# Optimization experiments

Measured on AMD Instinct MI355X. Metric: run time of the kernel, lower is better.

The kernel has to match this reference:

```python
import jax, jax.numpy as jnp
import numpy as np

BS, L, D = 128, 256, 512
H, DK = 2, 256  # heads, head dim
EPS_BN = 1e-5


def _lin(x, W, b):
    # torch Linear: W is (out, in)
    return jnp.einsum('...i,oi->...o', x, W) + b


def _bn(x, g, b, m, v):
    # eval-mode BatchNorm over channel axis = last axis of x
    return (x - m) * (g * jax.lax.rsqrt(v + EPS_BN)) + b


def setup_inputs() -> dict:
    key = jax.random.key(0)
    ks = iter(jax.random.split(key, 64))
    rn = lambda shape, s=0.02: jax.random.normal(next(ks), shape, dtype=jnp.float32) * s
    inp = {}
    inp['cap_emb'] = jax.random.normal(next(ks), (BS, L, D), dtype=jnp.float32)
    inp['lengths'] = jax.random.randint(next(ks), (BS,), 1, L + 1, dtype=jnp.int64 if jax.config.jax_enable_x64 else jnp.int32)
    # GA linears q,k,v
    for nm in ('Wq', 'Wk', 'Wv'):
        inp[nm] = rn((D, D))
    for nm in ('bq', 'bk', 'bv'):
        inp[nm] = rn((D,))
    inp['Wfq'] = rn((DK, DK)); inp['bfq'] = rn((DK,))
    inp['Wfk'] = rn((DK, DK)); inp['bfk'] = rn((DK,))
    inp['Wfg'] = rn((2 * DK, DK)); inp['bfg'] = rn((2 * DK,))
    # BatchNorm params (eval running stats)
    for pre in ('bn1', 'bn2', 'bn3'):
        inp[pre + '_g'] = 1.0 + rn((D,), 0.1)
        inp[pre + '_b'] = rn((D,), 0.1)
        inp[pre + '_m'] = rn((D,), 0.1)
        inp[pre + '_v'] = jax.random.uniform(next(ks), (D,), minval=0.5, maxval=1.5, dtype=jnp.float32)
    # Conv1d weights, torch layout (out, in, k)
    inp['Wc2'] = rn((D, D, 2)); inp['bc2'] = rn((D,))
    inp['Wc3'] = rn((D, D, 3)); inp['bc3'] = rn((D,))
    # MLP 512 -> 1024 -> 512
    inp['Wm1'] = rn((2 * D, D)); inp['bm1'] = rn((2 * D,))
    inp['Wm2'] = rn((D, 2 * D)); inp['bm2'] = rn((D,))
    return inp


def _forward(cap_emb, Wq, bq, Wk, bk, Wv, bv, Wfq, bfq, Wfk, bfk, Wfg, bfg,
             bn1_g, bn1_b, bn1_m, bn1_v, Wc2, bc2, bn2_g, bn2_b, bn2_m, bn2_v,
             Wc3, bc3, bn3_g, bn3_b, bn3_m, bn3_v, Wm1, bm1, Wm2, bm2, lengths):
    bs, seq, dim = cap_emb.shape
    # ---- GA: gated self-attention ----
    def split_heads(x):
        return x.reshape(bs, seq, H, DK).transpose(0, 2, 1, 3)  # [bs,h,seq,dk]
    q = split_heads(_lin(cap_emb, Wq, bq))
    k = split_heads(_lin(cap_emb, Wk, bk))
    v = split_heads(_lin(cap_emb, Wv, bv))
    G = _lin(q, Wfq, bfq) * _lin(k, Wfk, bfk)
    M = jax.nn.sigmoid(_lin(G, Wfg, bfg))  # [bs,h,seq,2*dk]
    qg = q * M[..., :DK]
    kg = k * M[..., DK:]
    # torch.div(..., rounding_mode='floor') == elementwise floor of scaled scores
    scores = jnp.floor(jnp.einsum('bhqd,bhkd->bhqk', qg, kg) / jnp.sqrt(jnp.float32(DK)))
    p_attn = jax.nn.softmax(scores, axis=-1)
    x = jnp.einsum('bhqk,bhkd->bhqd', p_attn, v)
    x = x.transpose(0, 2, 1, 3).reshape(bs, seq, dim)
    # BN over features (eval), dropout is identity in eval mode
    ga_emb = cap_emb + _bn(x, bn1_g, bn1_b, bn1_m, bn1_v)
    # ---- dual conv1d branches ----
    xc = cap_emb.transpose(0, 2, 1)  # [bs, D, L]
    dn = ('NCW', 'OIW', 'NCW')
    c2 = jax.lax.conv_general_dilated(xc, Wc2, window_strides=(2,), padding='VALID', dimension_numbers=dn) + bc2[None, :, None]
    c3 = jax.lax.conv_general_dilated(xc, Wc3, window_strides=(3,), padding='VALID', dimension_numbers=dn) + bc3[None, :, None]
    f2 = jax.nn.relu(_bn(c2.transpose(0, 2, 1), bn2_g, bn2_b, bn2_m, bn2_v))
    f3 = jax.nn.relu(_bn(c3.transpose(0, 2, 1), bn3_g, bn3_b, bn3_m, bn3_v))
    ga_jw = jnp.concatenate([ga_emb, f2, f3], axis=1)
    # ---- residual MLP (dropout identity in eval) ----
    hid = jax.nn.relu(_lin(ga_jw, Wm1, bm1))
    tex_emb = _lin(hid, Wm2, bm2) + ga_jw
    # ---- length-indexed gather ----
    idx = lengths.astype(jnp.int32) - 1
    out = tex_emb[jnp.arange(bs), idx]  # [bs, D]
    # l2norm
    norm = jnp.sqrt(jnp.sum(out * out, axis=-1, keepdims=True)) + 1e-8
    return out / norm


def reference(cap_emb, lengths, Wq, bq, Wk, bk, Wv, bv, Wfq, bfq, Wfk, bfk, Wfg, bfg,
              bn1_g, bn1_b, bn1_m, bn1_v, Wc2, bc2, bn2_g, bn2_b, bn2_m, bn2_v,
              Wc3, bc3, bn3_g, bn3_b, bn3_m, bn3_v, Wm1, bm1, Wm2, bm2):
    return _forward(cap_emb, Wq, bq, Wk, bk, Wv, bv, Wfq, bfq, Wfk, bfk, Wfg, bfg,
                    bn1_g, bn1_b, bn1_m, bn1_v, Wc2, bc2, bn2_g, bn2_b, bn2_m, bn2_v,
                    Wc3, bc3, bn3_g, bn3_b, bn3_m, bn3_v, Wm1, bm1, Wm2, bm2, lengths)
```

## Files before the change

### kernel.cpp

```cpp
#include <hip/hip_runtime.h>
#include <math.h>


typedef short bf16x8 __attribute__((ext_vector_type(8)));
typedef float f32x4 __attribute__((ext_vector_type(4)));
typedef short short4v __attribute__((ext_vector_type(4)));

__device__ __forceinline__ short f2bf(float x) {
    union { float f; unsigned u; } c; c.f = x;
    unsigned r = c.u + 0x7FFFu + ((c.u >> 16) & 1u);
    return (short)(r >> 16);
}
__device__ __forceinline__ float bf2f(short h) {
    union { float f; unsigned u; } c; c.u = ((unsigned)(unsigned short)h) << 16;
    return c.f;
}
__device__ __forceinline__ void glds16(const void* g, void* l) {
    __builtin_amdgcn_global_load_lds(
        (const __attribute__((address_space(1))) void*)g,
        (__attribute__((address_space(3))) void*)l, 16, 0, 0);
}

struct CastArgs {
    const float* src[3];
    short* dst[3];
    int n4[3];
};
__global__ __launch_bounds__(256) void cast_multi(CastArgs a)
{
    const int j = blockIdx.y;
    const float4* s = (const float4*)a.src[j];
    short* d = a.dst[j];
    const int n4 = a.n4[j];
    for (int i = blockIdx.x * 256 + threadIdx.x; i < n4; i += gridDim.x * 256) {
        float4 x = s[i];
        short4v h;
        h.x = f2bf(x.x); h.y = f2bf(x.y); h.z = f2bf(x.z); h.w = f2bf(x.w);
        *(short4v*)&d[i * 4] = h;
    }
}

__global__ __launch_bounds__(256)
void compose2(const float* __restrict__ Wq, const float* __restrict__ bq,
              const float* __restrict__ Wfq, const float* __restrict__ bfq,
              const float* __restrict__ Wk, const float* __restrict__ bk,
              const float* __restrict__ Wfk, const float* __restrict__ bfk,
              short* __restrict__ WaB, float* __restrict__ ba,
              short* __restrict__ WbB, float* __restrict__ bb)
{
    __shared__ float fq[256];
    __shared__ float redc[256];
    const int op = blockIdx.x;
    const int h = op >> 8, o = op & 255;
    const int t = threadIdx.x;
    const bool second = (blockIdx.y == 1);
    const float* W  = second ? Wk  : Wq;
    const float* bv = second ? bk  : bq;
    const float* F  = second ? Wfk : Wfq;
    const float* bf = second ? bfk : bfq;
    short* WB   = second ? WbB : WaB;
    float* bout = second ? bb  : ba;

    fq[t] = F[o * 256 + t];
    redc[t] = fq[t] * bv[h * 256 + t];
    __syncthreads();
    for (int s = 128; s > 0; s >>= 1) {
        if (t < s) redc[t] += redc[t + s];
        __syncthreads();
    }
    if (t == 0) bout[op] = redc[0] + bf[o];
    float s0 = 0.f, s1 = 0.f;
    for (int d = 0; d < 256; ++d) {
        const float f = fq[d];
        const float* wr = W + (size_t)(h * 256 + d) * 512;
        s0 += f * wr[t];
        s1 += f * wr[t + 256];
    }
    const size_t ro = (size_t)op * 512;
    WB[ro + t] = f2bf(s0);
    WB[ro + 256 + t] = f2bf(s1);
}

__global__ __launch_bounds__(256, 2)
void gemm_g(const short* __restrict__ capB,
            const short* __restrict__ WaB, const short* __restrict__ WbB,
            const float* __restrict__ ba, const float* __restrict__ bb,
            short* __restrict__ Gbuf)
{
    __shared__ short lds[2][12288];
    const int tid = threadIdx.x;
    const int bm = blockIdx.y * 128;
    const int bn = blockIdx.x * 128;
    const int z = blockIdx.z;
    const short* B1 = WaB + (size_t)z * 256 * 512;
    const short* B2 = WbB + (size_t)z * 256 * 512;

    const int lane = tid & 63;
    const int wr = (tid >> 7) & 1, wc = (tid >> 6) & 1;
    const int fr = lane & 15, kc = lane >> 4;
    const int r0 = tid >> 2;
    const int e0 = (((tid & 3) ^ ((r0 >> 1) & 3))) * 8;
    const int kce = (kc ^ ((fr >> 1) & 3)) * 8;

    auto stage = [&](int ph, int k0) {
        short* b = lds[ph];
        glds16(capB + (size_t)(bm + r0) * 512 + k0 + e0,      b + tid * 8);
        glds16(capB + (size_t)(bm + r0 + 64) * 512 + k0 + e0, b + (tid + 256) * 8);
        glds16(B1 + (size_t)(bn + r0) * 512 + k0 + e0,        b + 4096 + tid * 8);
        glds16(B1 + (size_t)(bn + r0 + 64) * 512 + k0 + e0,   b + 4096 + (tid + 256) * 8);
        glds16(B2 + (size_t)(bn + r0) * 512 + k0 + e0,        b + 8192 + tid * 8);
        glds16(B2 + (size_t)(bn + r0 + 64) * 512 + k0 + e0,   b + 8192 + (tid + 256) * 8);
    };

    f32x4 acc1[4][4], acc2[4][4];
#pragma unroll
    for (int i = 0; i < 4; ++i)
#pragma unroll
        for (int j = 0; j < 4; ++j) {
            acc1[i][j] = (f32x4){0.f, 0.f, 0.f, 0.f};
            acc2[i][j] = (f32x4){0.f, 0.f, 0.f, 0.f};
        }

    stage(0, 0);
    __syncthreads();
    for (int s = 0; s < 16; ++s) {
        if (s + 1 < 16) stage((s + 1) & 1, (s + 1) * 32);
        const short* b = lds[s & 1];
        bf16x8 ah[4], bh[4];
#pragma unroll
        for (int i = 0; i < 4; ++i)
            ah[i] = *(const bf16x8*)&b[(wr * 64 + i * 16 + fr) * 32 + kce];
#pragma unroll
        for (int i = 0; i < 4; ++i)
            bh[i] = *(const bf16x8*)&b[4096 + (wc * 64 + i * 16 + fr) * 32 + kce];
#pragma unroll
        for (int mi = 0; mi < 4; ++mi)
#pragma unroll
            for (int ni = 0; ni < 4; ++ni)
                acc1[mi][ni] = __builtin_amdgcn_mfma_f32_16x16x32_bf16(ah[mi], bh[ni], acc1[mi][ni], 0, 0, 0);
#pragma unroll
        for (int i = 0; i < 4; ++i)
            bh[i] = *(const bf16x8*)&b[8192 + (wc * 64 + i * 16 + fr) * 32 + kce];
#pragma unroll
        for (int mi = 0; mi < 4; ++mi)
#pragma unroll
            for (int ni = 0; ni < 4; ++ni)
                acc2[mi][ni] = __builtin_amdgcn_mfma_f32_16x16x32_bf16(ah[mi], bh[ni], acc2[mi][ni], 0, 0, 0);
        __syncthreads();
    }

#pragma unroll
    for (int mi = 0; mi < 4; ++mi) {
#pragma unroll
        for (int ni = 0; ni < 4; ++ni) {
#pragma unroll
            for (int r = 0; r < 4; ++r) {
                const int row = bm + wr * 64 + mi * 16 + kc * 4 + r;
                const int col = bn + wc * 64 + ni * 16 + fr;
                const float av  = acc1[mi][ni][r] + ba[z * 256 + col];
                const float lin = acc2[mi][ni][r] + bb[z * 256 + col];
                Gbuf[(size_t)row * 512 + z * 256 + col] = f2bf(lin * av);
            }
        }
    }
}

__global__ __launch_bounds__(256, 2)
void gemm_kg(const short* __restrict__ Gbuf,
             const short* __restrict__ Wfg2B, const float* __restrict__ bias,
             const short* __restrict__ capB,
             const short* __restrict__ WkB, const float* __restrict__ bk,
             const float* __restrict__ qg, float* __restrict__ scorep)
{
    __shared__ short lds[2][16384];
    __shared__ float sp[256];
    const int tid = threadIdx.x;
    const int bm = blockIdx.y * 128;
    const int bn = blockIdx.x * 128;
    const int z = blockIdx.z;
    const short* A1 = Gbuf + (size_t)z * 256;
    const short* B2 = WkB + (size_t)z * 256 * 512;

    const int lane = tid & 63;
    const int wr = (tid >> 7) & 1, wc = (tid >> 6) & 1;
    const int fr = lane & 15, kc = lane >> 4;
    const int r0 = tid >> 2;
    const int e0 = (((tid & 3) ^ ((r0 >> 1) & 3))) * 8;
    const int kce = (kc ^ ((fr >> 1) & 3)) * 8;

    auto stage = [&](int ph, int s) {
        short* b = lds[ph];
        const int k0 = s * 32;
        glds16(capB + (size_t)(bm + r0) * 512 + k0 + e0,      b + 8192 + tid * 8);
        glds16(capB + (size_t)(bm + r0 + 64) * 512 + k0 + e0, b + 8192 + (tid + 256) * 8);
        glds16(B2 + (size_t)(bn + r0) * 512 + k0 + e0,        b + 12288 + tid * 8);
        glds16(B2 + (size_t)(bn + r0 + 64) * 512 + k0 + e0,   b + 12288 + (tid + 256) * 8);
        if (s < 8) {
            glds16(A1 + (size_t)(bm + r0) * 512 + k0 + e0,        b + tid * 8);
            glds16(A1 + (size_t)(bm + r0 + 64) * 512 + k0 + e0,   b + (tid + 256) * 8);
            glds16(Wfg2B + (size_t)(bn + r0) * 256 + k0 + e0,     b + 4096 + tid * 8);
            glds16(Wfg2B + (size_t)(bn + r0 + 64) * 256 + k0 + e0, b + 4096 + (tid + 256) * 8);
        }
    };

    f32x4 acc1[4][4], acc2[4][4];
#pragma unroll
    for (int i = 0; i < 4; ++i)
#pragma unroll
        for (int j = 0; j < 4; ++j) {
            acc1[i][j] = (f32x4){0.f, 0.f, 0.f, 0.f};
            acc2[i][j] = (f32x4){0.f, 0.f, 0.f, 0.f};
        }

    stage(0, 0);
    __syncthreads();
    for (int s = 0; s < 16; ++s) {
        if (s + 1 < 16) stage((s + 1) & 1, s + 1);
        const short* b = lds[s & 1];
        bf16x8 ah[4], bh[4];
#pragma unroll
        for (int i = 0; i < 4; ++i)
            ah[i] = *(const bf16x8*)&b[8192 + (wr * 64 + i * 16 + fr) * 32 + kce];
#pragma unroll
        for (int i = 0; i < 4; ++i)
            bh[i] = *(const bf16x8*)&b[12288 + (wc * 64 + i * 16 + fr) * 32 + kce];
#pragma unroll
        for (int mi = 0; mi < 4; ++mi)
#pragma unroll
            for (int ni = 0; ni < 4; ++ni)
                acc2[mi][ni] = __builtin_amdgcn_mfma_f32_16x16x32_bf16(ah[mi], bh[ni], acc2[mi][ni], 0, 0, 0);
        if (s < 8) {
#pragma unroll
            for (int i = 0; i < 4; ++i)
                ah[i] = *(const bf16x8*)&b[(wr * 64 + i * 16 + fr) * 32 + kce];
#pragma unroll
            for (int i = 0; i < 4; ++i)
                bh[i] = *(const bf16x8*)&b[4096 + (wc * 64 + i * 16 + fr) * 32 + kce];
#pragma unroll
            for (int mi = 0; mi < 4; ++mi)
#pragma unroll
                for (int ni = 0; ni < 4; ++ni)
                    acc1[mi][ni] = __builtin_amdgcn_mfma_f32_16x16x32_bf16(ah[mi], bh[ni], acc1[mi][ni], 0, 0, 0);
        }
        __syncthreads();
    }

    float qgv[4];
    float pt[4][4];
    {
        const int b = bm >> 8;
#pragma unroll
        for (int ni = 0; ni < 4; ++ni)
            qgv[ni] = qg[b * 512 + z * 256 + bn + wc * 64 + ni * 16 + fr];
#pragma unroll
        for (int mi = 0; mi < 4; ++mi)
#pragma unroll
            for (int r = 0; r < 4; ++r) pt[mi][r] = 0.f;
    }

#pragma unroll
    for (int mi = 0; mi < 4; ++mi) {
#pragma unroll
        for (int ni = 0; ni < 4; ++ni) {
#pragma unroll
            for (int r = 0; r < 4; ++r) {
                const int col = bn + wc * 64 + ni * 16 + fr;
                const float v = acc1[mi][ni][r] + bias[col];
                const float e = acc2[mi][ni][r] + bk[z * 256 + col];
                const float kgv = e / (1.f + expf(-v));
                pt[mi][r] += kgv * qgv[ni];
            }
        }
    }

#pragma unroll
    for (int mi = 0; mi < 4; ++mi) {
#pragma unroll
        for (int r = 0; r < 4; ++r) {
            float p = pt[mi][r];
            p += __shfl_xor(p, 1);
            p += __shfl_xor(p, 2);
            p += __shfl_xor(p, 4);
            p += __shfl_xor(p, 8);
            if (fr == 0) {
                const int row_local = wr * 64 + mi * 16 + kc * 4 + r;
                sp[row_local * 2 + wc] = p;
            }
        }
    }
    __syncthreads();
    if (tid < 128) {
        const int row = bm + tid;
        const float s = sp[tid * 2] + sp[tid * 2 + 1];
        const int b = row >> 8, j = row & 255;
        scorep[((size_t)(b * 2 + z) * 256 + j) * 2 + blockIdx.x] = s;
    }
}

__global__ __launch_bounds__(256)
void qg_kernel(const float* __restrict__ cap,
               const short* __restrict__ Gbuf,
               const float* __restrict__ Wq, const float* __restrict__ bq,
               const float* __restrict__ Wfg, const float* __restrict__ bfg,
               const int* __restrict__ lengths, float* __restrict__ qg)
{
    __shared__ float cr[512];
    __shared__ float gs[256];
    const int b = blockIdx.x >> 1, h = blockIdx.x & 1;
    const int t = threadIdx.x;
    int r = lengths[b] - 1;
    if (r < 0) r = 0;
    if (r > 255) r = 255;
    const size_t base = ((size_t)b * 256 + r) * 512;
    cr[t] = cap[base + t];
    cr[t + 256] = cap[base + 256 + t];
    gs[t] = bf2f(Gbuf[base + h * 256 + t]);
    __syncthreads();
    const float4* wq4 = (const float4*)(Wq + (size_t)(h * 256 + t) * 512);
    float q = 0.f;
    for (int k4 = 0; k4 < 128; ++k4) {
        float4 w = wq4[k4];
        q += w.x * cr[k4 * 4 + 0] + w.y * cr[k4 * 4 + 1]
           + w.z * cr[k4 * 4 + 2] + w.w * cr[k4 * 4 + 3];
    }
    q += bq[h * 256 + t];
    const float4* w4 = (const float4*)(Wfg + (size_t)t * 256);
    float a = 0.f;
    for (int k4 = 0; k4 < 64; ++k4) {
        float4 w = w4[k4];
        a += w.x * gs[k4 * 4 + 0] + w.y * gs[k4 * 4 + 1]
           + w.z * gs[k4 * 4 + 2] + w.w * gs[k4 * 4 + 3];
    }
    a += bfg[t];
    qg[b * 512 + h * 256 + t] = q / (1.f + expf(-a));
}

__global__ __launch_bounds__(256)
void pbar_kernel(const float* __restrict__ scorep, const short* __restrict__ capB,
                 float* __restrict__ pbar)
{
    __shared__ float sc[512], red[512];
    const int b = blockIdx.y, cg = blockIdx.x;
    const int t = threadIdx.x;
#pragma unroll
    for (int i = 0; i < 2; ++i) {
        const int o = t + i * 256;
        const int h = o >> 8, j = o & 255;
        const size_t si = ((size_t)(b * 2 + h) * 256 + j) * 2;
        sc[o] = floorf((scorep[si] + scorep[si + 1]) * 0.0625f);
    }
    __syncthreads();
    red[t] = sc[t]; red[t + 256] = sc[t + 256];
    __syncthreads();
    for (int s = 128; s > 0; s >>= 1) {
        if (t < s) {
            red[t] = fmaxf(red[t], red[t + s]);
            red[256 + t] = fmaxf(red[256 + t], red[256 + t + s]);
        }
        __syncthreads();
    }
    const float mx0 = red[0], mx1 = red[256];
    __syncthreads();
    const float e0 = expf(sc[t] - mx0);
    const float e1 = expf(sc[t + 256] - mx1);
    red[t] = e0; red[t + 256] = e1;
    __syncthreads();
    for (int s = 128; s > 0; s >>= 1) {
        if (t < s) { red[t] += red[t + s]; red[256 + t] += red[256 + t + s]; }
        __syncthreads();
    }
    sc[t] = e0 / red[0];
    sc[t + 256] = e1 / red[256];
    __syncthreads();

    const int c = cg * 64 + (t & 63);
    const int jg = t >> 6;
    float a0 = 0.f, a1 = 0.f;
    for (int j = jg * 64; j < jg * 64 + 64; ++j) {
        const float cv = bf2f(capB[((size_t)(b * 256 + j)) * 512 + c]);
        a0 += sc[j] * cv;
        a1 += sc[256 + j] * cv;
    }
    red[t] = a0;
    __syncthreads();
    if (t < 64) {
        const float s0 = red[t] + red[t + 64] + red[t + 128] + red[t + 192];
        pbar[b * 1024 + cg * 64 + t] = s0;
    }
    __syncthreads();
    red[t] = a1;
    __syncthreads();
    if (t < 64) {
        const float s1 = red[t] + red[t + 64] + red[t + 128] + red[t + 192];
        pbar[b * 1024 + 512 + cg * 64 + t] = s1;
    }
}

__global__ __launch_bounds__(256)
void bnx_kernel(const float* __restrict__ pbar, const float* __restrict__ cap,
                const int* __restrict__ lengths,
                const float* __restrict__ Wv, const float* __restrict__ bv,
                const float* __restrict__ g1, const float* __restrict__ b1,
                const float* __restrict__ m1, const float* __restrict__ v1,
                float* __restrict__ xga)
{
    __shared__ float pb[1024];
    const int b = blockIdx.x;
    const int t = threadIdx.x;
    int r = lengths[b] - 1;
    if (r < 0) r = 0;
    if (r > 255) r = 255;
    const size_t base = ((size_t)b * 256 + r) * 512;
    pb[t] = pbar[b * 1024 + t];
    pb[t + 256] = pbar[b * 1024 + 256 + t];
    pb[t + 512] = pbar[b * 1024 + 512 + t];
    pb[t + 768] = pbar[b * 1024 + 768 + t];
    __syncthreads();
    float x0 = 0.f, x1 = 0.f;
    {
        const float4* w4 = (const float4*)(Wv + (size_t)t * 512);
        for (int k4 = 0; k4 < 128; ++k4) {
            float4 w = w4[k4];
            x0 += w.x * pb[k4 * 4 + 0] + w.y * pb[k4 * 4 + 1]
                + w.z * pb[k4 * 4 + 2] + w.w * pb[k4 * 4 + 3];
        }
        x0 += bv[t];
    }
    {
        const float4* w4 = (const float4*)(Wv + (size_t)(t + 256) * 512);
        for (int k4 = 0; k4 < 128; ++k4) {
            float4 w = w4[k4];
            x1 += w.x * pb[512 + k4 * 4 + 0] + w.y * pb[512 + k4 * 4 + 1]
                + w.z * pb[512 + k4 * 4 + 2] + w.w * pb[512 + k4 * 4 + 3];
        }
        x1 += bv[t + 256];
    }
    const int c0 = t, c1 = t + 256;
    const float s0 = g1[c0] / sqrtf(v1[c0] + 1e-5f);
    const float s1 = g1[c1] / sqrtf(v1[c1] + 1e-5f);
    xga[b * 512 + c0] = cap[base + c0] + (x0 - m1[c0]) * s0 + b1[c0];
    xga[b * 512 + c1] = cap[base + c1] + (x1 - m1[c1]) * s1 + b1[c1];
}

__global__ __launch_bounds__(256)
void mlp1(const float* __restrict__ xga, const float* __restrict__ W,
          const float* __restrict__ bias, float* __restrict__ hid)
{
    __shared__ float xs[16 * 512];
    const int r0 = blockIdx.y * 16;
    const int c0 = blockIdx.x * 64;
    for (int i = threadIdx.x; i < 2048; i += 256)
        ((float4*)xs)[i] = ((const float4*)(xga + (size_t)r0 * 512))[i];
    __syncthreads();
    const int col = c0 + (threadIdx.x & 63);
    const int rg = (threadIdx.x >> 6) * 4;
    float acc[4] = {0.f, 0.f, 0.f, 0.f};
    const float4* w4 = (const float4*)(W + (size_t)col * 512);
    for (int k4 = 0; k4 < 128; ++k4) {
        float4 w = w4[k4];
#pragma unroll
        for (int rr = 0; rr < 4; ++rr) {
            float4 x = *(const float4*)&xs[(rg + rr) * 512 + k4 * 4];
            acc[rr] += w.x * x.x + w.y * x.y + w.z * x.z + w.w * x.w;
        }
    }
    const float bb = bias[col];
#pragma unroll
    for (int rr = 0; rr < 4; ++rr)
        hid[(size_t)(r0 + rg + rr) * 1024 + col] = fmaxf(acc[rr] + bb, 0.f);
}

__global__ __launch_bounds__(256)
void mlp2(const float* __restrict__ hid, const float* __restrict__ W,
          const float* __restrict__ bias, const float* __restrict__ xga,
          float* __restrict__ tex)
{
    __shared__ float xs[16 * 1024];
    const int r0 = blockIdx.y * 16;
    const int c0 = blockIdx.x * 64;
    for (int i = threadIdx.x; i < 4096; i += 256)
        ((float4*)xs)[i] = ((const float4*)(hid + (size_t)r0 * 1024))[i];
    __syncthreads();
    const int col = c0 + (threadIdx.x & 63);
    const int rg = (threadIdx.x >> 6) * 4;
    float acc[4] = {0.f, 0.f, 0.f, 0.f};
    const float4* w4 = (const float4*)(W + (size_t)col * 1024);
    for (int k4 = 0; k4 < 256; ++k4) {
        float4 w = w4[k4];
#pragma unroll
        for (int rr = 0; rr < 4; ++rr) {
            float4 x = *(const float4*)&xs[(rg + rr) * 1024 + k4 * 4];
            acc[rr] += w.x * x.x + w.y * x.y + w.z * x.z + w.w * x.w;
        }
    }
    const float bb = bias[col];
#pragma unroll
    for (int rr = 0; rr < 4; ++rr) {
        const int row = r0 + rg + rr;
        tex[(size_t)row * 512 + col] = acc[rr] + bb + xga[(size_t)row * 512 + col];
    }
}

__global__ __launch_bounds__(256)
void norm_out(const float* __restrict__ tex, float* __restrict__ out)
{
    __shared__ float red[256];
    const int b = blockIdx.x;
    const int t = threadIdx.x;
    const float a = tex[b * 512 + t];
    const float c = tex[b * 512 + 256 + t];
    red[t] = a * a + c * c;
    __syncthreads();
    for (int s = 128; s > 0; s >>= 1) {
        if (t < s) red[t] += red[t + s];
        __syncthreads();
    }
    const float inv = 1.f / (sqrtf(red[0]) + 1e-8f);
    out[b * 512 + t] = a * inv;
    out[b * 512 + 256 + t] = c * inv;
}

extern "C" void kernel_launch(void* const* d_in, const int* in_sizes, int n_in,
                              void* d_out, int out_size, void* d_ws, size_t ws_size,
                              hipStream_t stream)
{
    const float* cap = (const float*)d_in[0];
    const int* lengths = (const int*)d_in[1];
    const float* Wq  = (const float*)d_in[2];
    const float* Wk  = (const float*)d_in[3];
    const float* Wv  = (const float*)d_in[4];
    const float* bq  = (const float*)d_in[5];
    const float* bk  = (const float*)d_in[6];
    const float* bv  = (const float*)d_in[7];
    const float* Wfq = (const float*)d_in[8];
    const float* bfq = (const float*)d_in[9];
    const float* Wfk = (const float*)d_in[10];
    const float* bfk = (const float*)d_in[11];
    const float* Wfg = (const float*)d_in[12];
    const float* bfg = (const float*)d_in[13];
    const float* g1  = (const float*)d_in[14];
    const float* b1  = (const float*)d_in[15];
    const float* m1  = (const float*)d_in[16];
    const float* v1  = (const float*)d_in[17];
    const float* Wm1 = (const float*)d_in[30];
    const float* bm1 = (const float*)d_in[31];
    const float* Wm2 = (const float*)d_in[32];
    const float* bm2 = (const float*)d_in[33];
    float* out = (float*)d_out;

    char* w = (char*)d_ws;
    const size_t MB = 1024 * 1024;
    short* capB = (short*)(w);
    short* Gbuf = (short*)(w + 32 * MB);
    char* wp = w + 64 * MB;
    short* WkB   = (short*)wp; wp += 524288;
    short* WaB   = (short*)wp; wp += 524288;
    short* WbB   = (short*)wp; wp += 524288;
    short* Wfg2B = (short*)wp; wp += 131072;
    float* ba     = (float*)wp; wp += 2048;
    float* bb     = (float*)wp; wp += 2048;
    float* qg     = (float*)wp; wp += 262144;
    float* scorep = (float*)wp; wp += 524288;
    float* pbar   = (float*)wp; wp += 524288;
    float* xga    = (float*)wp; wp += 262144;
    float* hid    = (float*)wp; wp += 524288;
    float* tex    = (float*)wp; wp += 262144;

    CastArgs ca;
    ca.src[0] = cap;          ca.dst[0] = capB;  ca.n4[0] = 4194304;
    ca.src[1] = Wk;           ca.dst[1] = WkB;   ca.n4[1] = 65536;
    ca.src[2] = Wfg + 65536;  ca.dst[2] = Wfg2B; ca.n4[2] = 16384;
    cast_multi<<<dim3(4096, 3), 256, 0, stream>>>(ca);

    compose2<<<dim3(512, 2), 256, 0, stream>>>(Wq, bq, Wfq, bfq, Wk, bk, Wfk, bfk,
                                               WaB, ba, WbB, bb);

    gemm_g<<<dim3(2, 256, 2), 256, 0, stream>>>(capB, WaB, WbB, ba, bb, Gbuf);

    qg_kernel<<<dim3(256), 256, 0, stream>>>(cap, Gbuf, Wq, bq, Wfg, bfg, lengths, qg);

    gemm_kg<<<dim3(2, 256, 2), 256, 0, stream>>>(Gbuf, Wfg2B, bfg + 256,
                                                 capB, WkB, bk, qg, scorep);

    pbar_kernel<<<dim3(8, 128), 256, 0, stream>>>(scorep, capB, pbar);
    bnx_kernel<<<dim3(128), 256, 0, stream>>>(pbar, cap, lengths, Wv, bv, g1, b1, m1, v1, xga);

    mlp1<<<dim3(16, 8), 256, 0, stream>>>(xga, Wm1, bm1, hid);
    mlp2<<<dim3(8, 8), 256, 0, stream>>>(hid, Wm2, bm2, xga, tex);
    norm_out<<<dim3(128), 256, 0, stream>>>(tex, out);
}
```

Baseline: 269.3 us.

## Fuse launches: merge prep, g-gemm with qg, pbar with bnx, MLP with norm

Cuts the pipeline from ten launches to five. The cast and weight-compose steps merge into one prep kernel. The qg computation runs as extra blocks inside the G GEMM and recomputes the needed G row itself from the composed weights, so it no longer waits on Gbuf. The pbar reduction is folded into the bnx kernel, now one block per batch. The two MLP layers and the l2 norm are fused into a single 32-block kernel, which removes the launch gaps and intermediate buffers but leaves much less parallelism in the pbar and MLP stages.

```diff
diff --git a/kernel.cpp b/kernel.cpp
--- a/kernel.cpp
+++ b/kernel.cpp
@@ -21,45 +21,42 @@
         (__attribute__((address_space(3))) void*)l, 16, 0, 0);
 }
 
-struct CastArgs {
+struct PrepArgs {
     const float* src[3];
     short* dst[3];
     int n4[3];
+    const float *Wq, *bq, *Wfq, *bfq, *Wk, *bk, *Wfk, *bfk;
+    short *WaB, *WbB;
+    float *ba, *bb;
 };
-__global__ __launch_bounds__(256) void cast_multi(CastArgs a)
+__global__ __launch_bounds__(256) void prep_kernel(PrepArgs a)
 {
-    const int j = blockIdx.y;
-    const float4* s = (const float4*)a.src[j];
-    short* d = a.dst[j];
-    const int n4 = a.n4[j];
-    for (int i = blockIdx.x * 256 + threadIdx.x; i < n4; i += gridDim.x * 256) {
-        float4 x = s[i];
-        short4v h;
-        h.x = f2bf(x.x); h.y = f2bf(x.y); h.z = f2bf(x.z); h.w = f2bf(x.w);
-        *(short4v*)&d[i * 4] = h;
-    }
-}
-
-__global__ __launch_bounds__(256)
-void compose2(const float* __restrict__ Wq, const float* __restrict__ bq,
-              const float* __restrict__ Wfq, const float* __restrict__ bfq,
-              const float* __restrict__ Wk, const float* __restrict__ bk,
-              const float* __restrict__ Wfk, const float* __restrict__ bfk,
-              short* __restrict__ WaB, float* __restrict__ ba,
-              short* __restrict__ WbB, float* __restrict__ bb)
-{
+    const int y = blockIdx.y;
+    const int t = threadIdx.x;
+    if (y < 3) {
+        const float4* s = (const float4*)a.src[y];
+        short* d = a.dst[y];
+        const int n4 = a.n4[y];
+        for (int i = blockIdx.x * 256 + t; i < n4; i += gridDim.x * 256) {
+            float4 x = s[i];
+            short4v h;
+            h.x = f2bf(x.x); h.y = f2bf(x.y); h.z = f2bf(x.z); h.w = f2bf(x.w);
+            *(short4v*)&d[i * 4] = h;
+        }
+        return;
+    }
+    if (blockIdx.x >= 512) return;
     __shared__ float fq[256];
     __shared__ float redc[256];
     const int op = blockIdx.x;
     const int h = op >> 8, o = op & 255;
-    const int t = threadIdx.x;
-    const bool second = (blockIdx.y == 1);
-    const float* W  = second ? Wk  : Wq;
-    const float* bv = second ? bk  : bq;
-    const float* F  = second ? Wfk : Wfq;
-    const float* bf = second ? bfk : bfq;
-    short* WB   = second ? WbB : WaB;
-    float* bout = second ? bb  : ba;
+    const bool second = (y == 4);
+    const float* W  = second ? a.Wk  : a.Wq;
+    const float* bv = second ? a.bk  : a.bq;
+    const float* F  = second ? a.Wfk : a.Wfq;
+    const float* bf = second ? a.bfk : a.bfq;
+    short* WB   = second ? a.WbB : a.WaB;
+    float* bout = second ? a.bb  : a.ba;
 
     fq[t] = F[o * 256 + t];
     redc[t] = fq[t] * bv[h * 256 + t];
@@ -81,17 +78,72 @@
     WB[ro + 256 + t] = f2bf(s1);
 }
 
-__global__ __launch_bounds__(256, 2)
-void gemm_g(const short* __restrict__ capB,
-            const short* __restrict__ WaB, const short* __restrict__ WbB,
-            const float* __restrict__ ba, const float* __restrict__ bb,
-            short* __restrict__ Gbuf)
+__global__ __launch_bounds__(256)
+void gemm_g_qg(const short* __restrict__ capB,
+               const short* __restrict__ WaB, const short* __restrict__ WbB,
+               const float* __restrict__ ba, const float* __restrict__ bb,
+               short* __restrict__ Gbuf,
+               const float* __restrict__ cap,
+               const float* __restrict__ Wq, const float* __restrict__ bq,
+               const float* __restrict__ Wfg, const float* __restrict__ bfg,
+               const int* __restrict__ lengths, float* __restrict__ qg)
 {
     __shared__ short lds[2][12288];
     const int tid = threadIdx.x;
-    const int bm = blockIdx.y * 128;
-    const int bn = blockIdx.x * 128;
-    const int z = blockIdx.z;
+
+    if (blockIdx.x < 256) {
+        float* cr = (float*)&lds[0][0];
+        float* gs = cr + 512;
+        const int b = blockIdx.x >> 1, h = blockIdx.x & 1;
+        const int t = tid;
+        int r = lengths[b] - 1;
+        if (r < 0) r = 0;
+        if (r > 255) r = 255;
+        const size_t base = ((size_t)b * 256 + r) * 512;
+        cr[t] = cap[base + t];
+        cr[t + 256] = cap[base + 256 + t];
+        __syncthreads();
+        {
+            const bf16x8* wa8 = (const bf16x8*)(WaB + (size_t)(h * 256 + t) * 512);
+            const bf16x8* wb8 = (const bf16x8*)(WbB + (size_t)(h * 256 + t) * 512);
+            float sa = 0.f, sb = 0.f;
+            for (int k8 = 0; k8 < 64; ++k8) {
+                bf16x8 wa = wa8[k8];
+                bf16x8 wb = wb8[k8];
+#pragma unroll
+                for (int j = 0; j < 8; ++j) {
+                    const float c = cr[k8 * 8 + j];
+                    sa += bf2f(wa[j]) * c;
+                    sb += bf2f(wb[j]) * c;
+                }
+            }
+            gs[t] = (sb + bb[h * 256 + t]) * (sa + ba[h * 256 + t]);
+        }
+        __syncthreads();
+        const float4* wq4 = (const float4*)(Wq + (size_t)(h * 256 + t) * 512);
+        float q = 0.f;
+        for (int k4 = 0; k4 < 128; ++k4) {
+            float4 w = wq4[k4];
+            q += w.x * cr[k4 * 4 + 0] + w.y * cr[k4 * 4 + 1]
+               + w.z * cr[k4 * 4 + 2] + w.w * cr[k4 * 4 + 3];
+        }
+        q += bq[h * 256 + t];
+        const float4* w4 = (const float4*)(Wfg + (size_t)t * 256);
+        float a = 0.f;
+        for (int k4 = 0; k4 < 64; ++k4) {
+            float4 w = w4[k4];
+            a += w.x * gs[k4 * 4 + 0] + w.y * gs[k4 * 4 + 1]
+               + w.z * gs[k4 * 4 + 2] + w.w * gs[k4 * 4 + 3];
+        }
+        a += bfg[t];
+        qg[b * 512 + h * 256 + t] = q / (1.f + expf(-a));
+        return;
+    }
+
+    const int gid = blockIdx.x - 256;
+    const int bn = (gid & 1) * 128;
+    const int bm = ((gid >> 1) & 255) * 128;
+    const int z = gid >> 9;
     const short* B1 = WaB + (size_t)z * 256 * 512;
     const short* B2 = WbB + (size_t)z * 256 * 512;
 
@@ -298,49 +350,15 @@
 }
 
 __global__ __launch_bounds__(256)
-void qg_kernel(const float* __restrict__ cap,
-               const short* __restrict__ Gbuf,
-               const float* __restrict__ Wq, const float* __restrict__ bq,
-               const float* __restrict__ Wfg, const float* __restrict__ bfg,
-               const int* __restrict__ lengths, float* __restrict__ qg)
+void pbar_bnx(const float* __restrict__ scorep, const short* __restrict__ capB,
+              const float* __restrict__ cap, const int* __restrict__ lengths,
+              const float* __restrict__ Wv, const float* __restrict__ bv,
+              const float* __restrict__ g1, const float* __restrict__ b1,
+              const float* __restrict__ m1, const float* __restrict__ v1,
+              float* __restrict__ xga)
 {
-    __shared__ float cr[512];
-    __shared__ float gs[256];
-    const int b = blockIdx.x >> 1, h = blockIdx.x & 1;
-    const int t = threadIdx.x;
-    int r = lengths[b] - 1;
-    if (r < 0) r = 0;
-    if (r > 255) r = 255;
-    const size_t base = ((size_t)b * 256 + r) * 512;
-    cr[t] = cap[base + t];
-    cr[t + 256] = cap[base + 256 + t];
-    gs[t] = bf2f(Gbuf[base + h * 256 + t]);
-    __syncthreads();
-    const float4* wq4 = (const float4*)(Wq + (size_t)(h * 256 + t) * 512);
-    float q = 0.f;
-    for (int k4 = 0; k4 < 128; ++k4) {
-        float4 w = wq4[k4];
-        q += w.x * cr[k4 * 4 + 0] + w.y * cr[k4 * 4 + 1]
-           + w.z * cr[k4 * 4 + 2] + w.w * cr[k4 * 4 + 3];
-    }
-    q += bq[h * 256 + t];
-    const float4* w4 = (const float4*)(Wfg + (size_t)t * 256);
-    float a = 0.f;
-    for (int k4 = 0; k4 < 64; ++k4) {
-        float4 w = w4[k4];
-        a += w.x * gs[k4 * 4 + 0] + w.y * gs[k4 * 4 + 1]
-           + w.z * gs[k4 * 4 + 2] + w.w * gs[k4 * 4 + 3];
-    }
-    a += bfg[t];
-    qg[b * 512 + h * 256 + t] = q / (1.f + expf(-a));
-}
-
-__global__ __launch_bounds__(256)
-void pbar_kernel(const float* __restrict__ scorep, const short* __restrict__ capB,
-                 float* __restrict__ pbar)
-{
-    __shared__ float sc[512], red[512];
-    const int b = blockIdx.y, cg = blockIdx.x;
+    __shared__ float sc[512], red[512], pb[1024];
+    const int b = blockIdx.x;
     const int t = threadIdx.x;
 #pragma unroll
     for (int i = 0; i < 2; ++i) {
@@ -373,49 +391,22 @@
     sc[t + 256] = e1 / red[256];
     __syncthreads();
 
-    const int c = cg * 64 + (t & 63);
-    const int jg = t >> 6;
-    float a0 = 0.f, a1 = 0.f;
-    for (int j = jg * 64; j < jg * 64 + 64; ++j) {
-        const float cv = bf2f(capB[((size_t)(b * 256 + j)) * 512 + c]);
-        a0 += sc[j] * cv;
-        a1 += sc[256 + j] * cv;
-    }
-    red[t] = a0;
-    __syncthreads();
-    if (t < 64) {
-        const float s0 = red[t] + red[t + 64] + red[t + 128] + red[t + 192];
-        pbar[b * 1024 + cg * 64 + t] = s0;
-    }
-    __syncthreads();
-    red[t] = a1;
-    __syncthreads();
-    if (t < 64) {
-        const float s1 = red[t] + red[t + 64] + red[t + 128] + red[t + 192];
-        pbar[b * 1024 + 512 + cg * 64 + t] = s1;
-    }
-}
-
-__global__ __launch_bounds__(256)
-void bnx_kernel(const float* __restrict__ pbar, const float* __restrict__ cap,
-                const int* __restrict__ lengths,
-                const float* __restrict__ Wv, const float* __restrict__ bv,
-                const float* __restrict__ g1, const float* __restrict__ b1,
-                const float* __restrict__ m1, const float* __restrict__ v1,
-                float* __restrict__ xga)
-{
-    __shared__ float pb[1024];
-    const int b = blockIdx.x;
-    const int t = threadIdx.x;
+    float a00 = 0.f, a01 = 0.f, a10 = 0.f, a11 = 0.f;
+    for (int j = 0; j < 256; ++j) {
+        const float p0 = sc[j], p1 = sc[256 + j];
+        const float cv0 = bf2f(capB[((size_t)(b * 256 + j)) * 512 + t]);
+        const float cv1 = bf2f(capB[((size_t)(b * 256 + j)) * 512 + 256 + t]);
+        a00 += p0 * cv0; a01 += p0 * cv1;
+        a10 += p1 * cv0; a11 += p1 * cv1;
+    }
+    pb[t] = a00; pb[256 + t] = a01;
+    pb[512 + t] = a10; pb[768 + t] = a11;
+    __syncthreads();
+
     int r = lengths[b] - 1;
     if (r < 0) r = 0;
     if (r > 255) r = 255;
     const size_t base = ((size_t)b * 256 + r) * 512;
-    pb[t] = pbar[b * 1024 + t];
-    pb[t + 256] = pbar[b * 1024 + 256 + t];
-    pb[t + 512] = pbar[b * 1024 + 512 + t];
-    pb[t + 768] = pbar[b * 1024 + 768 + t];
-    __syncthreads();
     float x0 = 0.f, x1 = 0.f;
     {
         const float4* w4 = (const float4*)(Wv + (size_t)t * 512);
@@ -443,81 +434,69 @@
 }
 
 __global__ __launch_bounds__(256)
-void mlp1(const float* __restrict__ xga, const float* __restrict__ W,
-          const float* __restrict__ bias, float* __restrict__ hid)
+void mlp_fused(const float* __restrict__ xga,
+               const float* __restrict__ Wm1, const float* __restrict__ bm1,
+               const float* __restrict__ Wm2, const float* __restrict__ bm2,
+               float* __restrict__ out)
 {
-    __shared__ float xs[16 * 512];
-    const int r0 = blockIdx.y * 16;
-    const int c0 = blockIdx.x * 64;
-    for (int i = threadIdx.x; i < 2048; i += 256)
-        ((float4*)xs)[i] = ((const float4*)(xga + (size_t)r0 * 512))[i];
-    __syncthreads();
-    const int col = c0 + (threadIdx.x & 63);
-    const int rg = (threadIdx.x >> 6) * 4;
-    float acc[4] = {0.f, 0.f, 0.f, 0.f};
-    const float4* w4 = (const float4*)(W + (size_t)col * 512);
-    for (int k4 = 0; k4 < 128; ++k4) {
-        float4 w = w4[k4];
-#pragma unroll
-        for (int rr = 0; rr < 4; ++rr) {
-            float4 x = *(const float4*)&xs[(rg + rr) * 512 + k4 * 4];
-            acc[rr] += w.x * x.x + w.y * x.y + w.z * x.z + w.w * x.w;
-        }
-    }
-    const float bb = bias[col];
-#pragma unroll
-    for (int rr = 0; rr < 4; ++rr)
-        hid[(size_t)(r0 + rg + rr) * 1024 + col] = fmaxf(acc[rr] + bb, 0.f);
-}
-
-__global__ __launch_bounds__(256)
-void mlp2(const float* __restrict__ hid, const float* __restrict__ W,
-          const float* __restrict__ bias, const float* __restrict__ xga,
-          float* __restrict__ tex)
-{
-    __shared__ float xs[16 * 1024];
-    const int r0 = blockIdx.y * 16;
-    const int c0 = blockIdx.x * 64;
-    for (int i = threadIdx.x; i < 4096; i += 256)
-        ((float4*)xs)[i] = ((const float4*)(hid + (size_t)r0 * 1024))[i];
-    __syncthreads();
-    const int col = c0 + (threadIdx.x & 63);
-    const int rg = (threadIdx.x >> 6) * 4;
-    float acc[4] = {0.f, 0.f, 0.f, 0.f};
-    const float4* w4 = (const float4*)(W + (size_t)col * 1024);
-    for (int k4 = 0; k4 < 256; ++k4) {
-        float4 w = w4[k4];
-#pragma unroll
-        for (int rr = 0; rr < 4; ++rr) {
-            float4 x = *(const float4*)&xs[(rg + rr) * 1024 + k4 * 4];
-            acc[rr] += w.x * x.x + w.y * x.y + w.z * x.z + w.w * x.w;
-        }
-    }
-    const float bb = bias[col];
-#pragma unroll
-    for (int rr = 0; rr < 4; ++rr) {
-        const int row = r0 + rg + rr;
-        tex[(size_t)row * 512 + col] = acc[rr] + bb + xga[(size_t)row * 512 + col];
-    }
-}
-
-__global__ __launch_bounds__(256)
-void norm_out(const float* __restrict__ tex, float* __restrict__ out)
-{
+    __shared__ float xs[4 * 512];
+    __shared__ float hs[4 * 1024];
+    __shared__ float tx[4 * 512];
     __shared__ float red[256];
-    const int b = blockIdx.x;
+    const int r0 = blockIdx.x * 4;
     const int t = threadIdx.x;
-    const float a = tex[b * 512 + t];
-    const float c = tex[b * 512 + 256 + t];
-    red[t] = a * a + c * c;
-    __syncthreads();
-    for (int s = 128; s > 0; s >>= 1) {
-        if (t < s) red[t] += red[t + s];
-        __syncthreads();
-    }
-    const float inv = 1.f / (sqrtf(red[0]) + 1e-8f);
-    out[b * 512 + t] = a * inv;
-    out[b * 512 + 256 + t] = c * inv;
+
+#pragma unroll
+    for (int i = 0; i < 8; ++i)
+        xs[t + i * 256] = xga[(size_t)r0 * 512 + t + i * 256];
+    __syncthreads();
+
+#pragma unroll
+    for (int i = 0; i < 16; ++i) {
+        const int idx = t + i * 256;
+        const int r = idx >> 10, col = idx & 1023;
+        const float4* w4 = (const float4*)(Wm1 + (size_t)col * 512);
+        const float* xr = xs + r * 512;
+        float acc = 0.f;
+        for (int k4 = 0; k4 < 128; ++k4) {
+            float4 w = w4[k4];
+            acc += w.x * xr[k4 * 4 + 0] + w.y * xr[k4 * 4 + 1]
+                 + w.z * xr[k4 * 4 + 2] + w.w * xr[k4 * 4 + 3];
+        }
+        hs[idx] = fmaxf(acc + bm1[col], 0.f);
+    }
+    __syncthreads();
+
+#pragma unroll
+    for (int i = 0; i < 8; ++i) {
+        const int idx = t + i * 256;
+        const int r = idx >> 9, col = idx & 511;
+        const float4* w4 = (const float4*)(Wm2 + (size_t)col * 1024);
+        const float* hr = hs + r * 1024;
+        float acc = 0.f;
+        for (int k4 = 0; k4 < 256; ++k4) {
+            float4 w = w4[k4];
+            acc += w.x * hr[k4 * 4 + 0] + w.y * hr[k4 * 4 + 1]
+                 + w.z * hr[k4 * 4 + 2] + w.w * hr[k4 * 4 + 3];
+        }
+        tx[idx] = acc + bm2[col] + xs[r * 512 + col];
+    }
+    __syncthreads();
+
+    for (int r = 0; r < 4; ++r) {
+        const float v0 = tx[r * 512 + t];
+        const float v1 = tx[r * 512 + 256 + t];
+        red[t] = v0 * v0 + v1 * v1;
+        __syncthreads();
+        for (int s = 128; s > 0; s >>= 1) {
+            if (t < s) red[t] += red[t + s];
+            __syncthreads();
+        }
+        const float inv = 1.f / (sqrtf(red[0]) + 1e-8f);
+        out[(size_t)(r0 + r) * 512 + t] = v0 * inv;
+        out[(size_t)(r0 + r) * 512 + 256 + t] = v1 * inv;
+        __syncthreads();
+    }
 }
 
 extern "C" void kernel_launch(void* const* d_in, const int* in_sizes, int n_in,
@@ -561,31 +540,25 @@
     float* bb     = (float*)wp; wp += 2048;
     float* qg     = (float*)wp; wp += 262144;
     float* scorep = (float*)wp; wp += 524288;
-    float* pbar   = (float*)wp; wp += 524288;
     float* xga    = (float*)wp; wp += 262144;
-    float* hid    = (float*)wp; wp += 524288;
-    float* tex    = (float*)wp; wp += 262144;
-
-    CastArgs ca;
-    ca.src[0] = cap;          ca.dst[0] = capB;  ca.n4[0] = 4194304;
-    ca.src[1] = Wk;           ca.dst[1] = WkB;   ca.n4[1] = 65536;
-    ca.src[2] = Wfg + 65536;  ca.dst[2] = Wfg2B; ca.n4[2] = 16384;
-    cast_multi<<<dim3(4096, 3), 256, 0, stream>>>(ca);
-
-    compose2<<<dim3(512, 2), 256, 0, stream>>>(Wq, bq, Wfq, bfq, Wk, bk, Wfk, bfk,
-                                               WaB, ba, WbB, bb);
-
-    gemm_g<<<dim3(2, 256, 2), 256, 0, stream>>>(capB, WaB, WbB, ba, bb, Gbuf);
-
-    qg_kernel<<<dim3(256), 256, 0, stream>>>(cap, Gbuf, Wq, bq, Wfg, bfg, lengths, qg);
+
+    PrepArgs pa;
+    pa.src[0] = cap;          pa.dst[0] = capB;  pa.n4[0] = 4194304;
+    pa.src[1] = Wk;           pa.dst[1] = WkB;   pa.n4[1] = 65536;
+    pa.src[2] = Wfg + 65536;  pa.dst[2] = Wfg2B; pa.n4[2] = 16384;
+    pa.Wq = Wq; pa.bq = bq; pa.Wfq = Wfq; pa.bfq = bfq;
+    pa.Wk = Wk; pa.bk = bk; pa.Wfk = Wfk; pa.bfk = bfk;
+    pa.WaB = WaB; pa.WbB = WbB; pa.ba = ba; pa.bb = bb;
+    prep_kernel<<<dim3(4096, 5), 256, 0, stream>>>(pa);
+
+    gemm_g_qg<<<dim3(1280), 256, 0, stream>>>(capB, WaB, WbB, ba, bb, Gbuf,
+                                              cap, Wq, bq, Wfg, bfg, lengths, qg);
 
     gemm_kg<<<dim3(2, 256, 2), 256, 0, stream>>>(Gbuf, Wfg2B, bfg + 256,
                                                  capB, WkB, bk, qg, scorep);
 
-    pbar_kernel<<<dim3(8, 128), 256, 0, stream>>>(scorep, capB, pbar);
-    bnx_kernel<<<dim3(128), 256, 0, stream>>>(pbar, cap, lengths, Wv, bv, g1, b1, m1, v1, xga);
-
-    mlp1<<<dim3(16, 8), 256, 0, stream>>>(xga, Wm1, bm1, hid);
-    mlp2<<<dim3(8, 8), 256, 0, stream>>>(hid, Wm2, bm2, xga, tex);
-    norm_out<<<dim3(128), 256, 0, stream>>>(tex, out);
-}
+    pbar_bnx<<<dim3(128), 256, 0, stream>>>(scorep, capB, cap, lengths,
+                                            Wv, bv, g1, b1, m1, v1, xga);
+
+    mlp_fused<<<dim3(32), 256, 0, stream>>>(xga, Wm1, bm1, Wm2, bm2, out);
+}
```

After: 679.3 us. 152% more time.
